# Optimization experiments

Hardware: AMD Instinct MI355X
Metric: run time of the kernel (lower is better)

The kernel has to match this reference:

```python
import jax, jax.numpy as jnp
import numpy as np

B, D, H, K = 65536, 256, 256, 11
TEMP = 1.0
EPS = 1e-8  # torch cosine_similarity eps


def _gelu(v):
    return jax.nn.gelu(v, approximate=False)  # torch nn.GELU default is exact


def setup_inputs() -> dict:
    key = jax.random.key(0)
    ks = jax.random.split(key, 9)
    s_d = 1.0 / np.sqrt(D)
    s_h = 1.0 / np.sqrt(H)
    return {
        "x": jax.random.normal(ks[0], (B, D), jnp.float32),
        # K transform MLPs, stacked: D->H (gelu) ->D
        "Tw1": jax.random.normal(ks[1], (K, D, H), jnp.float32) * s_d,
        "Tb1": jax.random.normal(ks[2], (K, H), jnp.float32) * 0.01,
        "Tw2": jax.random.normal(ks[3], (K, H, D), jnp.float32) * s_h,
        "Tb2": jax.random.normal(ks[4], (K, D), jnp.float32) * 0.01,
        # encoder MLP: D->H (gelu) ->H
        "Ew1": jax.random.normal(ks[5], (D, H), jnp.float32) * s_d,
        "Eb1": jax.random.normal(ks[6], (H,), jnp.float32) * 0.01,
        "Ew2": jax.random.normal(ks[7], (H, H), jnp.float32) * s_h,
        "Eb2": jax.random.normal(ks[8], (H,), jnp.float32) * 0.01,
    }


def reference(x, Tw1, Tb1, Tw2, Tb2, Ew1, Eb1, Ew2, Eb2):
    def enc(h):  # [..., D] -> [..., H]; dropout is identity at inference
        return _gelu(h @ Ew1 + Eb1) @ Ew2 + Eb2

    # batched transforms: [K, B, D]
    tx = _gelu(jnp.einsum('bd,kdh->kbh', x, Tw1) + Tb1[:, None, :])
    tx = jnp.einsum('kbh,khd->kbd', tx, Tw2) + Tb2[:, None, :]

    z = enc(x)        # [B, H]
    zt = enc(tx)      # [K, B, H]

    nz = jnp.linalg.norm(z, axis=-1)    # [B]
    nzt = jnp.linalg.norm(zt, axis=-1)  # [K, B]

    # exp(cos(z, z_k) / T)  -> [K, B]
    sim_z = jnp.exp(jnp.einsum('bh,kbh->kb', z, zt)
                    / jnp.maximum(nz[None, :] * nzt, EPS) / TEMP)
    # exp(cos(z_l, z_k) / T) -> [K, K, B]
    S = jnp.exp(jnp.einsum('lbh,kbh->lkb', zt, zt)
                / jnp.maximum(nzt[:, None, :] * nzt[None, :, :], EPS) / TEMP)
    diag = jnp.diagonal(S, axis1=0, axis2=1).T  # [K, B]
    neg = S.sum(axis=0) - diag                  # sum over l != k

    scores = jnp.log(sim_z / (sim_z + neg))     # [K, B]
    return -scores.sum(axis=0)                  # [B]
```

## Files before the change

### kernel.cpp

```cpp
#include <hip/hip_runtime.h>
#include <hip/hip_bf16.h>
#include <stdint.h>

#define BTOT  65536
#define KTR   11
#define NSLOT 12

typedef __attribute__((ext_vector_type(8))) short bf16x8_t;
typedef __attribute__((ext_vector_type(4))) float f32x4_t;

__device__ __forceinline__ int act_addr(int m, int n) {
    return m * 256 + ((((n >> 3) + m) & 31) << 3) + (n & 7);
}

__device__ __forceinline__ float gelu_fast(float x) {
    float x2 = x * x;
    float t2 = 2.3022083f * x * fmaf(0.044715f, x2, 1.0f);
    float e  = exp2f(-t2);
    return x * __builtin_amdgcn_rcpf(1.0f + e);
}

__global__ void cast_x_kernel(const float* __restrict__ x, __hip_bfloat16* __restrict__ xb) {
    int i = (blockIdx.x * 256 + threadIdx.x) * 4;
    float4 v = *(const float4*)(x + i);
    union { __hip_bfloat16 h[4]; uint64_t u; } o;
    o.h[0] = __float2bfloat16(v.x);
    o.h[1] = __float2bfloat16(v.y);
    o.h[2] = __float2bfloat16(v.z);
    o.h[3] = __float2bfloat16(v.w);
    *(uint64_t*)(xb + i) = o.u;
}

__global__ void transpose_cast_kernel(const float* __restrict__ in,
                                      __hip_bfloat16* __restrict__ out,
                                      int R, int C) {
    __shared__ float tile[32][33];
    int tpc = C >> 5;
    int tr = (blockIdx.x / tpc) << 5;
    int tc = (blockIdx.x % tpc) << 5;
    const float* bi = in + (size_t)blockIdx.y * R * C;
    __hip_bfloat16* bo = out + (size_t)blockIdx.y * R * C;
    int lx = threadIdx.x & 31, ly = threadIdx.x >> 5;
    #pragma unroll
    for (int r = 0; r < 32; r += 8)
        tile[ly + r][lx] = bi[(size_t)(tr + ly + r) * C + tc + lx];
    __syncthreads();
    #pragma unroll
    for (int r = 0; r < 32; r += 8)
        bo[(size_t)(tc + ly + r) * R + tr + lx] = __float2bfloat16(tile[lx][ly + r]);
}

__global__ void fuse_w_kernel(const __hip_bfloat16* __restrict__ Ew1t,
                              const __hip_bfloat16* __restrict__ Tw2b,
                              __hip_bfloat16* __restrict__ Wft)
{
    __shared__ __align__(16) __hip_bfloat16 bt[64 * 256];
    const int tid  = threadIdx.x;
    const int wave = tid >> 6, lane = tid & 63;
    const int lr = lane & 15, q = lane >> 4;
    const int k  = blockIdx.y;
    const int h0 = blockIdx.x << 6;
    const __hip_bfloat16* src = Tw2b + (size_t)k * 65536;

    #pragma unroll
    for (int i = 0; i < 8; ++i) {
        int lin = i * 256 + tid;
        int r = lin >> 5, g = lin & 31;
        bf16x8_t v = *(const bf16x8_t*)(src + (size_t)(h0 + r) * 256 + g * 8);
        *(bf16x8_t*)(bt + act_addr(r, g * 8)) = v;
    }
    __syncthreads();

    const int wc = wave << 6;
    f32x4_t acc[4][4];
    #pragma unroll
    for (int mt = 0; mt < 4; ++mt)
        #pragma unroll
        for (int nt = 0; nt < 4; ++nt)
            acc[mt][nt] = (f32x4_t){0.f, 0.f, 0.f, 0.f};

    #pragma unroll 1
    for (int kc = 0; kc < 8; ++kc) {
        const int kof = (kc << 5) + (q << 3);
        bf16x8_t a[4], b[4];
        #pragma unroll
        for (int mt = 0; mt < 4; ++mt)
            a[mt] = *(const bf16x8_t*)(Ew1t + (size_t)(wc + (mt << 4) + lr) * 256 + kof);
        #pragma unroll
        for (int nt = 0; nt < 4; ++nt)
            b[nt] = *(const bf16x8_t*)(bt + act_addr((nt << 4) + lr, kof));
        #pragma unroll
        for (int mt = 0; mt < 4; ++mt)
            #pragma unroll
            for (int nt = 0; nt < 4; ++nt)
                acc[mt][nt] = __builtin_amdgcn_mfma_f32_16x16x32_bf16(a[mt], b[nt], acc[mt][nt], 0, 0, 0);
    }

    __hip_bfloat16* dst = Wft + (size_t)k * 65536;
    #pragma unroll
    for (int mt = 0; mt < 4; ++mt)
        #pragma unroll
        for (int nt = 0; nt < 4; ++nt) {
            const int h = h0 + (nt << 4) + lr;
            #pragma unroll
            for (int r = 0; r < 4; ++r) {
                const int j = wc + (mt << 4) + (q << 2) + r;
                dst[(size_t)j * 256 + h] = __float2bfloat16(acc[mt][nt][r]);
            }
        }
}

__global__ void fuse_b_kernel(const float* __restrict__ Tb2,
                              const float* __restrict__ Ew1,
                              const float* __restrict__ Eb1,
                              float* __restrict__ bf)
{
    const int k = blockIdx.x, j = threadIdx.x;
    float s = Eb1[j];
    #pragma unroll 4
    for (int d = 0; d < 256; ++d)
        s = fmaf(Tb2[k * 256 + d], Ew1[d * 256 + j], s);
    bf[k * 256 + j] = s;
}

__device__ __forceinline__ void mfma_part(const __hip_bfloat16* act,
                                          const __hip_bfloat16* __restrict__ Wt,
                                          const float* __restrict__ bias,
                                          f32x4_t acc[4][4], int lr, int q, int wc)
{
    #pragma unroll
    for (int mt = 0; mt < 4; ++mt) {
        const float4 bv = *(const float4*)(bias + wc + (mt << 4) + (q << 2));
        #pragma unroll
        for (int nt = 0; nt < 4; ++nt)
            acc[mt][nt] = (f32x4_t){bv.x, bv.y, bv.z, bv.w};
    }

    bf16x8_t a[4];
    #pragma unroll
    for (int mt = 0; mt < 4; ++mt)
        a[mt] = *(const bf16x8_t*)(Wt + (size_t)(wc + (mt << 4) + lr) * 256 + (q << 3));

    #pragma unroll 1
    for (int kc = 0; kc < 8; ++kc) {
        const int kof = (kc << 5) + (q << 3);
        bf16x8_t an[4];
        if (kc < 7) {
            #pragma unroll
            for (int mt = 0; mt < 4; ++mt)
                an[mt] = *(const bf16x8_t*)(Wt + (size_t)(wc + (mt << 4) + lr) * 256 + kof + 32);
        }
        bf16x8_t b[4];
        #pragma unroll
        for (int nt = 0; nt < 4; ++nt)
            b[nt] = *(const bf16x8_t*)(act + act_addr((nt << 4) + lr, kof));
        #pragma unroll
        for (int mt = 0; mt < 4; ++mt)
            #pragma unroll
            for (int nt = 0; nt < 4; ++nt)
                acc[mt][nt] = __builtin_amdgcn_mfma_f32_16x16x32_bf16(a[mt], b[nt], acc[mt][nt], 0, 0, 0);
        if (kc < 7) {
            #pragma unroll
            for (int mt = 0; mt < 4; ++mt) a[mt] = an[mt];
        }
    }
}

template<bool DO_GELU>
__device__ __forceinline__ void ep_part(__hip_bfloat16* act, f32x4_t acc[4][4],
                                        int lr, int q, int wc)
{
    #pragma unroll
    for (int mt = 0; mt < 4; ++mt) {
        const int nbase = wc + (mt << 4) + (q << 2);
        #pragma unroll
        for (int nt = 0; nt < 4; ++nt) {
            const int row = (nt << 4) + lr;
            union { __hip_bfloat16 h[4]; uint64_t u; } o;
            #pragma unroll
            for (int r = 0; r < 4; ++r) {
                float v = acc[mt][nt][r];
                if (DO_GELU) v = gelu_fast(v);
                o.h[r] = __float2bfloat16(v);
            }
            *(uint64_t*)(act + act_addr(row, nbase)) = o.u;
        }
    }
}

__launch_bounds__(256, 2)
__global__ void chain_kernel(const __hip_bfloat16* __restrict__ xb,
                             const __hip_bfloat16* __restrict__ Tw1t,
                             const float* __restrict__ Tb1,
                             const __hip_bfloat16* __restrict__ Wft,
                             const float* __restrict__ bfb,
                             const __hip_bfloat16* __restrict__ Ew1t,
                             const float* __restrict__ Eb1,
                             const __hip_bfloat16* __restrict__ Ew2t,
                             const float* __restrict__ Eb2,
                             __hip_bfloat16* __restrict__ zbuf,
                             int b0)
{
    __shared__ __align__(16) __hip_bfloat16 actA[64 * 256];
    __shared__ __align__(16) __hip_bfloat16 actB[64 * 256];
    const int tid  = threadIdx.x;
    const int wave = tid >> 6, lane = tid & 63;
    const int lr = lane & 15, q = lane >> 4, wc = wave << 6;
    const int pair = blockIdx.y;
    const int tile = blockIdx.x;
    const int s0 = pair * 2, s1 = s0 + 1;
    const bool zp = (pair == 5);

    #pragma unroll
    for (int i = 0; i < 8; ++i) {
        int lin = i * 256 + tid;
        int r = lin >> 5, g = lin & 31;
        bf16x8_t v = *(const bf16x8_t*)(xb + (size_t)(b0 + tile * 64 + r) * 256 + g * 8);
        *(bf16x8_t*)(actA + act_addr(r, g * 8)) = v;
        *(bf16x8_t*)(actB + act_addr(r, g * 8)) = v;
    }
    __syncthreads();

    const __hip_bfloat16* WA0 = Tw1t + (size_t)s0 * 65536;
    const __hip_bfloat16* WA1 = Wft  + (size_t)s0 * 65536;
    const float* BA0 = Tb1 + s0 * 256;
    const float* BA1 = bfb + s0 * 256;
    const __hip_bfloat16* WB0 = zp ? Ew1t : Tw1t + (size_t)s1 * 65536;
    const __hip_bfloat16* WB1 = zp ? Ew2t : Wft  + (size_t)s1 * 65536;
    const float* BB0 = zp ? Eb1 : Tb1 + s1 * 256;
    const float* BB1 = zp ? Eb2 : bfb + s1 * 256;

    f32x4_t accA[4][4], accB[4][4];

    mfma_part(actA, WA0, BA0, accA, lr, q, wc);
    __syncthreads();
    mfma_part(actB, WB0, BB0, accB, lr, q, wc);
    ep_part<true>(actA, accA, lr, q, wc);
    __syncthreads();
    mfma_part(actA, WA1, BA1, accA, lr, q, wc);
    ep_part<true>(actB, accB, lr, q, wc);
    __syncthreads();
    mfma_part(actB, WB1, BB1, accB, lr, q, wc);
    ep_part<true>(actA, accA, lr, q, wc);
    __syncthreads();
    mfma_part(actA, Ew2t, Eb2, accA, lr, q, wc);
    if (zp) ep_part<false>(actB, accB, lr, q, wc);
    else    ep_part<true >(actB, accB, lr, q, wc);
    __syncthreads();
    if (!zp) mfma_part(actB, Ew2t, Eb2, accB, lr, q, wc);
    ep_part<false>(actA, accA, lr, q, wc);
    __syncthreads();
    if (!zp) {
        ep_part<false>(actB, accB, lr, q, wc);
        __syncthreads();
    }

    __hip_bfloat16* d0 = zbuf + (size_t)(tile * NSLOT + s0) * (64 * 256);
    __hip_bfloat16* d1 = zbuf + (size_t)(tile * NSLOT + s1) * (64 * 256);
    #pragma unroll
    for (int i = 0; i < 8; ++i) {
        int lin = i * 256 + tid;
        int r = lin >> 5, g = lin & 31;
        bf16x8_t v0 = *(const bf16x8_t*)(actA + act_addr(r, g * 8));
        __builtin_nontemporal_store(v0, (bf16x8_t*)(d0 + lin * 8));
        bf16x8_t v1 = *(const bf16x8_t*)(actB + act_addr(r, g * 8));
        __builtin_nontemporal_store(v1, (bf16x8_t*)(d1 + lin * 8));
    }
}

#define ROW_BODY(V, I)                                                        \
    {                                                                         \
        f32x4_t acc = (f32x4_t){0.f, 0.f, 0.f, 0.f};                          \
        _Pragma("unroll")                                                     \
        for (int kc = 0; kc < 8; ++kc)                                        \
            acc = __builtin_amdgcn_mfma_f32_16x16x32_bf16(V[kc], V[kc], acc, 0, 0, 0); \
        _Pragma("unroll")                                                     \
        for (int rr = 0; rr < 4; ++rr)                                        \
            Gw[wave][(q << 2) + rr][lr] = acc[rr];                            \
        float term = 0.f;                                                     \
        if (lane < 11) {                                                      \
            const int k = lane;                                               \
            float nr[NSLOT];                                                  \
            _Pragma("unroll")                                                 \
            for (int l = 0; l < NSLOT; ++l)                                   \
                nr[l] = __builtin_amdgcn_rcpf(fmaxf(sqrtf(Gw[wave][l][l]), 1e-4f)); \
            const float nrk = nr[k];                                          \
            float neg = 0.f;                                                  \
            _Pragma("unroll")                                                 \
            for (int l = 0; l < KTR; ++l)                                     \
                if (l != k)                                                   \
                    neg += __expf(Gw[wave][l][k] * nr[l] * nrk);              \
            float cz = Gw[wave][KTR][k] * nr[KTR] * nrk;                      \
            term = __logf(__expf(cz) + neg) - cz;                             \
        }                                                                     \
        term += __shfl_xor(term, 1);                                          \
        term += __shfl_xor(term, 2);                                          \
        term += __shfl_xor(term, 4);                                          \
        term += __shfl_xor(term, 8);                                          \
        if (lane == 0) out[b0 + r0 + (I)] = term;                             \
    }

__launch_bounds__(256, 4)
__global__ void reduce_kernel(const __hip_bfloat16* __restrict__ zbuf,
                              float* __restrict__ out, int b0)
{
    __shared__ float Gw[4][16][17];
    const int tid  = threadIdx.x;
    const int wave = tid >> 6, lane = tid & 63;
    const int lr = lane & 15, q = lane >> 4;
    const int slot = lr < NSLOT ? lr : NSLOT - 1;

    const int r0   = (blockIdx.x * 4 + wave) * 8;
    const int tile = r0 >> 6, rloc = r0 & 63;
    const __hip_bfloat16* zr = zbuf + (size_t)tile * (NSLOT * 64 * 256)
                             + (size_t)slot * (64 * 256) + rloc * 256 + (q << 3);

    bf16x8_t va[8], vb[8];
    #pragma unroll
    for (int kc = 0; kc < 8; ++kc)
        va[kc] = __builtin_nontemporal_load((const bf16x8_t*)(zr + kc * 32));

    #pragma unroll 1
    for (int i2 = 0; i2 < 4; ++i2) {
        const int ie = i2 * 2;
        {
            const __hip_bfloat16* zn = zr + (ie + 1) * 256;
            #pragma unroll
            for (int kc = 0; kc < 8; ++kc)
                vb[kc] = __builtin_nontemporal_load((const bf16x8_t*)(zn + kc * 32));
            ROW_BODY(va, ie)
        }
        {
            if (ie + 2 < 8) {
                const __hip_bfloat16* zn = zr + (ie + 2) * 256;
                #pragma unroll
                for (int kc = 0; kc < 8; ++kc)
                    va[kc] = __builtin_nontemporal_load((const bf16x8_t*)(zn + kc * 32));
            }
            ROW_BODY(vb, ie + 1)
        }
    }
}

extern "C" void kernel_launch(void* const* d_in, const int* in_sizes, int n_in,
                              void* d_out, int out_size, void* d_ws, size_t ws_size,
                              hipStream_t stream)
{
    const float* x   = (const float*)d_in[0];
    const float* Tw1 = (const float*)d_in[1];
    const float* Tb1 = (const float*)d_in[2];
    const float* Tw2 = (const float*)d_in[3];
    const float* Tb2 = (const float*)d_in[4];
    const float* Ew1 = (const float*)d_in[5];
    const float* Eb1 = (const float*)d_in[6];
    const float* Ew2 = (const float*)d_in[7];
    const float* Eb2 = (const float*)d_in[8];
    float* out = (float*)d_out;

    char* ws = (char*)d_ws;
    const size_t off_xb   = 0;
    const size_t off_tw1  = off_xb   + (size_t)BTOT * 256 * 2;
    const size_t off_wf   = off_tw1  + (size_t)KTR * 65536 * 2;
    const size_t off_ew1  = off_wf   + (size_t)KTR * 65536 * 2;
    const size_t off_ew2  = off_ew1  + (size_t)65536 * 2;
    const size_t off_tw2b = off_ew2  + (size_t)65536 * 2;
    const size_t off_bf   = off_tw2b + (size_t)KTR * 65536 * 2;
    const size_t off_z    = off_bf   + (size_t)KTR * 256 * 4;

    __hip_bfloat16* xb   = (__hip_bfloat16*)(ws + off_xb);
    __hip_bfloat16* Tw1t = (__hip_bfloat16*)(ws + off_tw1);
    __hip_bfloat16* Wft  = (__hip_bfloat16*)(ws + off_wf);
    __hip_bfloat16* Ew1t = (__hip_bfloat16*)(ws + off_ew1);
    __hip_bfloat16* Ew2t = (__hip_bfloat16*)(ws + off_ew2);
    __hip_bfloat16* Tw2b = (__hip_bfloat16*)(ws + off_tw2b);
    float*          bfb  = (float*)(ws + off_bf);
    __hip_bfloat16* zbuf = (__hip_bfloat16*)(ws + off_z);

    long long zbytes = (long long)ws_size - (long long)off_z;
    long long rows_cap = zbytes > 0 ? zbytes / ((long long)NSLOT * 256 * 2) : 0;
    int chunk = (int)((rows_cap / 128) * 128);
    if (chunk > BTOT / 4) chunk = BTOT / 4;
    if (chunk < 128) chunk = 128;

    cast_x_kernel<<<dim3(BTOT * 256 / 1024), 256, 0, stream>>>(x, xb);
    cast_x_kernel<<<dim3(KTR * 65536 / 1024), 256, 0, stream>>>(Tw2, Tw2b);
    transpose_cast_kernel<<<dim3(64, KTR), 256, 0, stream>>>(Tw1, Tw1t, 256, 256);
    transpose_cast_kernel<<<dim3(64, 1),   256, 0, stream>>>(Ew1, Ew1t, 256, 256);
    transpose_cast_kernel<<<dim3(64, 1),   256, 0, stream>>>(Ew2, Ew2t, 256, 256);
    fuse_b_kernel<<<dim3(KTR), 256, 0, stream>>>(Tb2, Ew1, Eb1, bfb);
    fuse_w_kernel<<<dim3(4, KTR), 256, 0, stream>>>(Ew1t, Tw2b, Wft);

    for (int b0 = 0; b0 < BTOT; b0 += chunk) {
        int rows = (BTOT - b0 < chunk) ? (BTOT - b0) : chunk;
        chain_kernel<<<dim3(rows / 64, NSLOT / 2), 256, 0, stream>>>(
            xb, Tw1t, Tb1, Wft, bfb, Ew1t, Eb1, Ew2t, Eb2, zbuf, b0);
        reduce_kernel<<<dim3(rows / 32), 256, 0, stream>>>(zbuf, out, b0);
    }
}
```

Baseline: 843.0 us.

## Split chain kernel into two wave groups, each owning one slot chain

Doubles the chain kernel block to 512 threads. Each group of four waves now owns one of the two interleaved slot chains and its own LDS activation buffer, where before a single set of waves alternated between both chains. The intent is to overlap one group's MFMA phase with the other group's epilogue across barriers and to halve per-wave accumulator registers. In exchange the block gets larger, launch bounds change, and each group idles at barriers while the other group works.

```diff
diff --git a/kernel.cpp b/kernel.cpp
--- a/kernel.cpp
+++ b/kernel.cpp
@@ -188,7 +188,7 @@
     }
 }
 
-__launch_bounds__(256, 2)
+__launch_bounds__(512, 2)
 __global__ void chain_kernel(const __hip_bfloat16* __restrict__ xb,
                              const __hip_bfloat16* __restrict__ Tw1t,
                              const float* __restrict__ Tb1,
@@ -205,15 +205,18 @@
     __shared__ __align__(16) __hip_bfloat16 actB[64 * 256];
     const int tid  = threadIdx.x;
     const int wave = tid >> 6, lane = tid & 63;
-    const int lr = lane & 15, q = lane >> 4, wc = wave << 6;
+    const int lr = lane & 15, q = lane >> 4;
+    const int grp = wave >> 2;
+    const int wc  = (wave & 3) << 6;
     const int pair = blockIdx.y;
     const int tile = blockIdx.x;
     const int s0 = pair * 2, s1 = s0 + 1;
     const bool zp = (pair == 5);
-
-    #pragma unroll
-    for (int i = 0; i < 8; ++i) {
-        int lin = i * 256 + tid;
+    __hip_bfloat16* act = grp ? actB : actA;
+
+    #pragma unroll
+    for (int i = 0; i < 4; ++i) {
+        int lin = i * 512 + tid;
         int r = lin >> 5, g = lin & 31;
         bf16x8_t v = *(const bf16x8_t*)(xb + (size_t)(b0 + tile * 64 + r) * 256 + g * 8);
         *(bf16x8_t*)(actA + act_addr(r, g * 8)) = v;
@@ -221,45 +224,50 @@
     }
     __syncthreads();
 
-    const __hip_bfloat16* WA0 = Tw1t + (size_t)s0 * 65536;
-    const __hip_bfloat16* WA1 = Wft  + (size_t)s0 * 65536;
-    const float* BA0 = Tb1 + s0 * 256;
-    const float* BA1 = bfb + s0 * 256;
-    const __hip_bfloat16* WB0 = zp ? Ew1t : Tw1t + (size_t)s1 * 65536;
-    const __hip_bfloat16* WB1 = zp ? Ew2t : Wft  + (size_t)s1 * 65536;
-    const float* BB0 = zp ? Eb1 : Tb1 + s1 * 256;
-    const float* BB1 = zp ? Eb2 : bfb + s1 * 256;
-
-    f32x4_t accA[4][4], accB[4][4];
-
-    mfma_part(actA, WA0, BA0, accA, lr, q, wc);
-    __syncthreads();
-    mfma_part(actB, WB0, BB0, accB, lr, q, wc);
-    ep_part<true>(actA, accA, lr, q, wc);
-    __syncthreads();
-    mfma_part(actA, WA1, BA1, accA, lr, q, wc);
-    ep_part<true>(actB, accB, lr, q, wc);
-    __syncthreads();
-    mfma_part(actB, WB1, BB1, accB, lr, q, wc);
-    ep_part<true>(actA, accA, lr, q, wc);
-    __syncthreads();
-    mfma_part(actA, Ew2t, Eb2, accA, lr, q, wc);
-    if (zp) ep_part<false>(actB, accB, lr, q, wc);
-    else    ep_part<true >(actB, accB, lr, q, wc);
-    __syncthreads();
-    if (!zp) mfma_part(actB, Ew2t, Eb2, accB, lr, q, wc);
-    ep_part<false>(actA, accA, lr, q, wc);
-    __syncthreads();
-    if (!zp) {
-        ep_part<false>(actB, accB, lr, q, wc);
-        __syncthreads();
-    }
+    const __hip_bfloat16 *W0, *W1, *W2;
+    const float *B0, *B1, *B2;
+    if (grp == 0) {
+        W0 = Tw1t + (size_t)s0 * 65536; B0 = Tb1 + s0 * 256;
+        W1 = Wft  + (size_t)s0 * 65536; B1 = bfb + s0 * 256;
+        W2 = Ew2t;                      B2 = Eb2;
+    } else if (!zp) {
+        W0 = Tw1t + (size_t)s1 * 65536; B0 = Tb1 + s1 * 256;
+        W1 = Wft  + (size_t)s1 * 65536; B1 = bfb + s1 * 256;
+        W2 = Ew2t;                      B2 = Eb2;
+    } else {
+        W0 = Ew1t; B0 = Eb1;
+        W1 = Ew2t; B1 = Eb2;
+        W2 = nullptr; B2 = nullptr;
+    }
+
+    f32x4_t acc[4][4];
+
+    if (!grp) mfma_part(act, W0, B0, acc, lr, q, wc);
+    __syncthreads();
+    if (!grp) ep_part<true>(act, acc, lr, q, wc);
+    else      mfma_part(act, W0, B0, acc, lr, q, wc);
+    __syncthreads();
+    if (!grp) mfma_part(act, W1, B1, acc, lr, q, wc);
+    else      ep_part<true>(act, acc, lr, q, wc);
+    __syncthreads();
+    if (!grp) ep_part<true>(act, acc, lr, q, wc);
+    else      mfma_part(act, W1, B1, acc, lr, q, wc);
+    __syncthreads();
+    if (!grp) mfma_part(act, W2, B2, acc, lr, q, wc);
+    else if (zp) ep_part<false>(act, acc, lr, q, wc);
+    else         ep_part<true >(act, acc, lr, q, wc);
+    __syncthreads();
+    if (!grp) ep_part<false>(act, acc, lr, q, wc);
+    else if (!zp) mfma_part(act, W2, B2, acc, lr, q, wc);
+    __syncthreads();
+    if (grp && !zp) ep_part<false>(act, acc, lr, q, wc);
+    __syncthreads();
 
     __hip_bfloat16* d0 = zbuf + (size_t)(tile * NSLOT + s0) * (64 * 256);
     __hip_bfloat16* d1 = zbuf + (size_t)(tile * NSLOT + s1) * (64 * 256);
     #pragma unroll
-    for (int i = 0; i < 8; ++i) {
-        int lin = i * 256 + tid;
+    for (int i = 0; i < 4; ++i) {
+        int lin = i * 512 + tid;
         int r = lin >> 5, g = lin & 31;
         bf16x8_t v0 = *(const bf16x8_t*)(actA + act_addr(r, g * 8));
         __builtin_nontemporal_store(v0, (bf16x8_t*)(d0 + lin * 8));
@@ -392,7 +400,7 @@
 
     for (int b0 = 0; b0 < BTOT; b0 += chunk) {
         int rows = (BTOT - b0 < chunk) ? (BTOT - b0) : chunk;
-        chain_kernel<<<dim3(rows / 64, NSLOT / 2), 256, 0, stream>>>(
+        chain_kernel<<<dim3(rows / 64, NSLOT / 2), 512, 0, stream>>>(
             xb, Tw1t, Tb1, Wft, bfb, Ew1t, Eb1, Ew2t, Eb2, zbuf, b0);
         reduce_kernel<<<dim3(rows / 32), 256, 0, stream>>>(zbuf, out, b0);
     }
```

After: 902.4 us. +7.0%, slower.
